# Performance work log

Hardware: AMD Instinct MI355X
Metric: run time of the kernel (lower is better)

Reference implementation:

```python
import jax, jax.numpy as jnp
import numpy as np

N, E = 50000, 800000
F_IN, F_OUT, H = 128, 16, 8
NEG_SLOPE = 0.2  # PyG GATConv default
EPS = 1e-5       # LayerNorm eps


def setup_inputs() -> dict:
    key = jax.random.key(0)
    ks = jax.random.split(key, 8)
    x = jax.random.normal(ks[0], (N, F_IN), dtype=jnp.float32)
    edge_index = jax.random.randint(ks[1], (2, E), 0, N, dtype=jnp.int32)
    s_in = 1.0 / np.sqrt(F_IN)
    s_f = 1.0 / np.sqrt(F_OUT)
    W = jax.random.normal(ks[2], (F_IN, H * F_OUT), dtype=jnp.float32) * s_in
    att_src = jax.random.normal(ks[3], (H, F_OUT), dtype=jnp.float32) * s_f
    att_dst = jax.random.normal(ks[4], (H, F_OUT), dtype=jnp.float32) * s_f
    bias = jnp.zeros((H * F_OUT,), dtype=jnp.float32)
    gamma = jnp.ones((H * F_OUT,), dtype=jnp.float32)
    beta = jnp.zeros((H * F_OUT,), dtype=jnp.float32)
    return {"x": x, "edge_index": edge_index, "W": W, "att_src": att_src,
            "att_dst": att_dst, "bias": bias, "gamma": gamma, "beta": beta}


def _gat_layer(x, edge_index, W, att_src, att_dst, bias, gamma, beta):
    n = x.shape[0]
    # add self loops (PyG GATConv default add_self_loops=True)
    loop = jnp.arange(n, dtype=edge_index.dtype)
    src = jnp.concatenate([edge_index[0], loop])  # message source j
    dst = jnp.concatenate([edge_index[1], loop])  # message target i

    xp = (x @ W).reshape(n, H, F_OUT)                      # [N,H,F]
    a_src = jnp.einsum('nhf,hf->nh', xp, att_src)          # [N,H]
    a_dst = jnp.einsum('nhf,hf->nh', xp, att_dst)          # [N,H]

    e = a_src[src] + a_dst[dst]                            # [E+N,H]
    e = jax.nn.leaky_relu(e, NEG_SLOPE)
    # softmax over incoming edges per destination node
    m = jax.ops.segment_max(e, dst, num_segments=n)        # [N,H]
    e = jnp.exp(e - m[dst])
    z = jax.ops.segment_sum(e, dst, num_segments=n)        # [N,H]
    alpha = e / jnp.where(z[dst] > 0, z[dst], 1.0)         # [E+N,H]

    msg = alpha[:, :, None] * xp[src]                      # [E+N,H,F]
    out = jax.ops.segment_sum(msg, dst, num_segments=n)    # [N,H,F]
    out = out.reshape(n, H * F_OUT) + bias

    # LayerNorm over feature dim
    mu = out.mean(axis=-1, keepdims=True)
    var = out.var(axis=-1, keepdims=True)
    return (out - mu) * jax.lax.rsqrt(var + EPS) * gamma + beta


def reference(x, edge_index, W, att_src, att_dst, bias, gamma, beta):
    return _gat_layer(x, edge_index, W, att_src, att_dst, bias, gamma, beta)
```

## Files before the change

kernel.cpp:

```cpp
#include <hip/hip_runtime.h>
#include <math.h>

#define F_IN 128
#define NHD 8
#define FEAT 128
#define NEG_SLOPE 0.2f
#define LN_EPS 1e-5f
#define BSH 7
#define BMSK 127
#define NPQ 32
#define CAP 48
#define EPB 2048
#define NBMAX 512

typedef __bf16 v8bf __attribute__((ext_vector_type(8)));
typedef __bf16 v2bf __attribute__((ext_vector_type(2)));
typedef float f32x4 __attribute__((ext_vector_type(4)));

__global__ __launch_bounds__(256) void k_wt(const float* __restrict__ W,
                                            __bf16* __restrict__ WT) {
    int idx = blockIdx.x * 256 + threadIdx.x;
    int k = idx >> 7, c = idx & 127;
    WT[c * 128 + k] = (__bf16)W[idx];
}

__global__ __launch_bounds__(512) void k_fused(const float* __restrict__ x,
                                               const __bf16* __restrict__ WT,
                                               const float* __restrict__ att_src,
                                               const float* __restrict__ att_dst,
                                               __bf16* __restrict__ xp16,
                                               float* __restrict__ a_src,
                                               float* __restrict__ a_dst,
                                               const int* __restrict__ src,
                                               const int* __restrict__ dst,
                                               unsigned int* __restrict__ sorted_g,
                                               int* __restrict__ runptr,
                                               int n, int E, int Ga) {
    __shared__ __bf16 xs[32][136];
    if ((int)blockIdx.x < Ga) {
        __shared__ int lcnt[NBMAX];
        __shared__ int loff[NBMAX + 1];
        __shared__ unsigned int sorted_l[EPB];
        __shared__ int wtot[8], wexcl[8];
        int NB = (n + BMSK) >> BSH;
        int tid = threadIdx.x, lane = tid & 63, wid = tid >> 6;
        long base0 = (long)blockIdx.x * EPB;
        long total = (long)E + n;
        if (tid < NB) lcnt[tid] = 0;
        __syncthreads();

        int s0[4], d0[4];
        bool val[4];
        long e0 = base0 + (long)tid * 4;
        if (e0 + 3 < E) {
            int4 sv = *(const int4*)(src + e0);
            int4 dv = *(const int4*)(dst + e0);
            s0[0] = sv.x; s0[1] = sv.y; s0[2] = sv.z; s0[3] = sv.w;
            d0[0] = dv.x; d0[1] = dv.y; d0[2] = dv.z; d0[3] = dv.w;
            val[0] = val[1] = val[2] = val[3] = true;
        } else {
#pragma unroll
            for (int j = 0; j < 4; ++j) {
                long e = e0 + j;
                val[j] = (e < total);
                s0[j] = d0[j] = 0;
                if (val[j]) {
                    if (e < E) { s0[j] = src[e]; d0[j] = dst[e]; }
                    else { s0[j] = d0[j] = (int)(e - E); }
                }
            }
        }
#pragma unroll
        for (int j = 0; j < 4; ++j)
            if (val[j]) atomicAdd(&lcnt[d0[j] >> BSH], 1);
        __syncthreads();

        int v = (tid < NB) ? lcnt[tid] : 0;
        int xx = v;
#pragma unroll
        for (int o = 1; o < 64; o <<= 1) {
            int t2 = __shfl_up(xx, o);
            if (lane >= o) xx += t2;
        }
        if (lane == 63) wtot[wid] = xx;
        __syncthreads();
        if (wid == 0 && lane < 8) {
            int s = wtot[lane];
            int y = s;
#pragma unroll
            for (int o = 1; o < 8; o <<= 1) {
                int t2 = __shfl_up(y, o);
                if (lane >= o) y += t2;
            }
            wexcl[lane] = y - s;
        }
        __syncthreads();
        int excl = wexcl[wid] + xx - v;
        if (tid < NB) loff[tid] = excl;
        if (tid == NB - 1) loff[NB] = excl + v;
        __syncthreads();
        if (tid < NB) lcnt[tid] = loff[tid];
        __syncthreads();
#pragma unroll
        for (int j = 0; j < 4; ++j) {
            if (val[j]) {
                int b = d0[j] >> BSH;
                int pos = atomicAdd(&lcnt[b], 1);
                sorted_l[pos] = ((unsigned)s0[j] << BSH) | (unsigned)(d0[j] & BMSK);
            }
        }
        __syncthreads();
        int tv = loff[NB];
        for (int i = tid; i < tv; i += 512)
            sorted_g[base0 + i] = sorted_l[i];
        if (tid <= NB) runptr[(long)blockIdx.x * (NBMAX + 1) + tid] = loff[tid];
    } else {
        int gb = blockIdx.x - Ga;
        int tid = threadIdx.x;
        int rowbase = gb * 32;
        {
            int i4 = tid;
#pragma unroll
            for (int rep = 0; rep < 2; ++rep, i4 += 512) {
                int r = i4 >> 5, c4 = i4 & 31;
                int gr = rowbase + r; if (gr > n - 1) gr = n - 1;
                float4 xv = *(const float4*)(x + (long)gr * 128 + c4 * 4);
                __bf16* p = &xs[r][c4 * 4];
                p[0] = (__bf16)xv.x; p[1] = (__bf16)xv.y;
                p[2] = (__bf16)xv.z; p[3] = (__bf16)xv.w;
            }
        }
        __syncthreads();
        int wv = tid >> 6;
        int lane = tid & 63;
        int m = lane & 15, quad = lane >> 4;
        int colbase = wv * 16;
        const __bf16* wcol = WT + (colbase + m) * 128;
        v8bf wf[4];
#pragma unroll
        for (int kk = 0; kk < 4; ++kk)
            wf[kk] = *(const v8bf*)(wcol + kk * 32 + quad * 8);
        float ws = att_src[colbase + m];
        float wd = att_dst[colbase + m];
#pragma unroll
        for (int t = 0; t < 2; ++t) {
            int rb = t * 16;
            f32x4 acc = {0.f, 0.f, 0.f, 0.f};
#pragma unroll
            for (int kk = 0; kk < 4; ++kk) {
                v8bf a = *(const v8bf*)(&xs[rb + m][kk * 32 + quad * 8]);
                acc = __builtin_amdgcn_mfma_f32_16x16x32_bf16(a, wf[kk], acc, 0, 0, 0);
            }
#pragma unroll
            for (int r = 0; r < 4; ++r) {
                int row = rowbase + rb + quad * 4 + r;
                float ts = acc[r] * ws;
                float td = acc[r] * wd;
#pragma unroll
                for (int o = 1; o < 16; o <<= 1) {
                    ts += __shfl_xor(ts, o);
                    td += __shfl_xor(td, o);
                }
                if (row < n) {
                    xp16[(long)row * 128 + colbase + m] = (__bf16)acc[r];
                    if (m == 0) {
                        a_src[row * 8 + wv] = ts;
                        a_dst[row * 8 + wv] = td;
                    }
                }
            }
        }
    }
}

__global__ __launch_bounds__(256) void k_ba(const unsigned int* __restrict__ sorted_g,
                                            const int* __restrict__ runptr,
                                            const float* __restrict__ a_src,
                                            const float* __restrict__ a_dst,
                                            const __bf16* __restrict__ xp16,
                                            const float* __restrict__ bias,
                                            const float* __restrict__ gamma,
                                            const float* __restrict__ beta,
                                            const int* __restrict__ src,
                                            const int* __restrict__ dst,
                                            float* __restrict__ out, int n, int E, int Ga) {
    __shared__ int slds[NPQ * CAP];
    __shared__ int lc[NPQ];
    __shared__ float adst_s[NPQ * NHD];
    int b = blockIdx.x >> 2;
    int q = blockIdx.x & 3;
    int tid = threadIdx.x;
    int node0 = (b << BSH) + q * NPQ;
    if (tid < NPQ) lc[tid] = 0;
    if (tid < NPQ * NHD) {
        int nd = node0 + (tid >> 3);
        adst_s[tid] = (nd < n) ? a_dst[nd * NHD + (tid & 7)] : 0.f;
    }
    __syncthreads();

    int qlo = q * NPQ;
    for (int blk = tid; blk < Ga; blk += 256) {
        const int* rp = runptr + (long)blk * (NBMAX + 1) + b;
        int st = rp[0], en = rp[1];
        const unsigned int* sg = sorted_g + (long)blk * EPB;
        for (int i = st; i < en; ++i) {
            unsigned int u = sg[i];
            int dl = (int)(u & BMSK) - qlo;
            if ((unsigned)dl < NPQ) {
                int p = atomicAdd(&lc[dl], 1);
                if (p < CAP) slds[dl * CAP + p] = (int)(u >> BSH);
            }
        }
    }
    __syncthreads();
    if (tid < NPQ) {
        int cc = lc[tid]; if (cc > CAP) cc = CAP;
        int pad = (cc + 7) & ~7; if (pad > CAP) pad = CAP;
        for (int p = cc; p < pad; ++p) slds[tid * CAP + p] = 0;
    }
    __syncthreads();

    int lane = tid & 63, wv = tid >> 6;
    int h = lane & 7, j8 = lane >> 3;
    float2 bs = *(const float2*)(bias + 2 * lane);
    float2 g  = *(const float2*)(gamma + 2 * lane);
    float2 bt = *(const float2*)(beta + 2 * lane);

    for (int i = wv; i < NPQ; i += 4) {
        int node = node0 + i;
        if (node >= n) break;
        int cnt = lc[i];
        float acc0 = 0.f, acc1 = 0.f, inv;

        if (cnt <= CAP) {
            const int* row = slds + i * CAP;
            float b_h = adst_s[i * NHD + h];
            float zacc = 0.f;
            for (int base = 0; base < cnt; base += 8) {
                int s_my = row[base + j8];
                float e = a_src[s_my * NHD + h] + b_h;
                e = e > 0.f ? e : NEG_SLOPE * e;
                float w_my = (base + j8 < cnt) ? __expf(e) : 0.f;
                zacc += w_my;
                int ss[8];
#pragma unroll
                for (int j = 0; j < 8; ++j) ss[j] = row[base + j];
                float2 vals[8];
#pragma unroll
                for (int j = 0; j < 8; ++j) {
                    v2bf p = *(const v2bf*)(xp16 + (long)ss[j] * FEAT + 2 * lane);
                    vals[j] = make_float2((float)p[0], (float)p[1]);
                }
#pragma unroll
                for (int j = 0; j < 8; ++j) {
                    float w = __shfl(w_my, j * 8 + j8);
                    acc0 = fmaf(w, vals[j].x, acc0);
                    acc1 = fmaf(w, vals[j].y, acc1);
                }
            }
            zacc += __shfl_xor(zacc, 8);
            zacc += __shfl_xor(zacc, 16);
            zacc += __shfl_xor(zacc, 32);
            float z = __shfl(zacc, j8);
            inv = 1.f / z;
        } else {
            float b_h = a_dst[node * NHD + j8];
            float z = 0.f;
            {
                float e = a_src[node * NHD + j8] + b_h;
                e = e > 0.f ? e : NEG_SLOPE * e;
                float w = __expf(e);
                z += w;
                v2bf p = *(const v2bf*)(xp16 + (long)node * FEAT + 2 * lane);
                acc0 = fmaf(w, (float)p[0], acc0);
                acc1 = fmaf(w, (float)p[1], acc1);
            }
            for (int base = 0; base < E; base += 64) {
                int e = base + lane;
                int sv = 0;
                bool mt = false;
                if (e < E) { mt = (dst[e] == node); if (mt) sv = src[e]; }
                unsigned long long mask = __ballot(mt);
                while (mask) {
                    int bl = __ffsll(mask) - 1;
                    mask &= mask - 1;
                    int s = __shfl(sv, bl);
                    float ee = a_src[s * NHD + j8] + b_h;
                    ee = ee > 0.f ? ee : NEG_SLOPE * ee;
                    float w = __expf(ee);
                    z += w;
                    v2bf p = *(const v2bf*)(xp16 + (long)s * FEAT + 2 * lane);
                    acc0 = fmaf(w, (float)p[0], acc0);
                    acc1 = fmaf(w, (float)p[1], acc1);
                }
            }
            inv = 1.f / z;
        }

        float v0 = acc0 * inv + bs.x;
        float v1 = acc1 * inv + bs.y;
        float ssum = v0 + v1;
        float ssq = v0 * v0 + v1 * v1;
#pragma unroll
        for (int o = 32; o > 0; o >>= 1) {
            ssum += __shfl_xor(ssum, o);
            ssq += __shfl_xor(ssq, o);
        }
        float mu = ssum * (1.0f / FEAT);
        float var = ssq * (1.0f / FEAT) - mu * mu;
        float rs = rsqrtf(var + LN_EPS);
        float2 o2;
        o2.x = (v0 - mu) * rs * g.x + bt.x;
        o2.y = (v1 - mu) * rs * g.y + bt.y;
        *(float2*)(out + (long)node * FEAT + 2 * lane) = o2;
    }
}

extern "C" void kernel_launch(void* const* d_in, const int* in_sizes, int n_in,
                              void* d_out, int out_size, void* d_ws, size_t ws_size,
                              hipStream_t stream) {
    const float* x = (const float*)d_in[0];
    const int* edge_index = (const int*)d_in[1];
    const float* W = (const float*)d_in[2];
    const float* att_src = (const float*)d_in[3];
    const float* att_dst = (const float*)d_in[4];
    const float* bias = (const float*)d_in[5];
    const float* gamma = (const float*)d_in[6];
    const float* beta = (const float*)d_in[7];
    float* out = (float*)d_out;

    int n = in_sizes[0] / F_IN;
    int E = in_sizes[1] / 2;
    const int* src = edge_index;
    const int* dst = edge_index + E;
    int NB = (n + BMSK) >> BSH;
    int Ga = (E + n + EPB - 1) / EPB;

    char* ws = (char*)d_ws;
    __bf16* WT   = (__bf16*)ws;                    ws += (size_t)128 * 128 * 2;
    __bf16* xp16 = (__bf16*)ws;                    ws += (size_t)n * FEAT * 2;
    float* a_src = (float*)ws;                     ws += (size_t)n * NHD * 4;
    float* a_dst = (float*)ws;                     ws += (size_t)n * NHD * 4;
    unsigned int* sorted_g = (unsigned int*)ws;    ws += (size_t)Ga * EPB * 4;
    int* runptr  = (int*)ws;                       ws += (size_t)Ga * (NBMAX + 1) * 4;

    k_wt<<<64, 256, 0, stream>>>(W, WT);
    int Gg = (n + 31) / 32;
    k_fused<<<Ga + Gg, 512, 0, stream>>>(x, WT, att_src, att_dst, xp16, a_src, a_dst,
                                         src, dst, sorted_g, runptr, n, E, Ga);
    k_ba<<<NB * 4, 256, 0, stream>>>(sorted_g, runptr, a_src, a_dst, xp16,
                                     bias, gamma, beta, src, dst, out, n, E, Ga);
}
```

Baseline: 180.9 us.

## Stage GEMM output in LDS, widen row tiles, split aggregation blocks finer

The projection part of the fused kernel now handles 64 rows per block and stages the bf16 result in shared memory. From there it writes xp16 with coalesced 16-byte stores and computes the attention dot products directly, replacing the per-element strided stores and shuffle reductions. The aggregation kernel halves nodes per block (NPQ 16, 8 quarters per bucket) for more parallelism. It also precomputes all edge weights and a_src gathers up front, so the loads are independent of each other. The costs are more blocks each rescanning runptr, which doubles the bucket-scan traffic, and higher register use from the unrolled arrays.

```diff
diff --git a/kernel.cpp b/kernel.cpp
--- a/kernel.cpp
+++ b/kernel.cpp
@@ -8,10 +8,11 @@
 #define LN_EPS 1e-5f
 #define BSH 7
 #define BMSK 127
-#define NPQ 32
+#define NPQ 16
 #define CAP 48
 #define EPB 2048
 #define NBMAX 512
+#define GROWS 64
 
 typedef __bf16 v8bf __attribute__((ext_vector_type(8)));
 typedef __bf16 v2bf __attribute__((ext_vector_type(2)));
@@ -36,12 +37,13 @@
                                                unsigned int* __restrict__ sorted_g,
                                                int* __restrict__ runptr,
                                                int n, int E, int Ga) {
-    __shared__ __bf16 xs[32][136];
+    extern __shared__ char smem[];
     if ((int)blockIdx.x < Ga) {
-        __shared__ int lcnt[NBMAX];
-        __shared__ int loff[NBMAX + 1];
-        __shared__ unsigned int sorted_l[EPB];
-        __shared__ int wtot[8], wexcl[8];
+        int* lcnt = (int*)smem;
+        int* loff = lcnt + NBMAX;
+        unsigned int* sorted_l = (unsigned int*)(loff + NBMAX + 1);
+        int* wtot = (int*)(sorted_l + EPB);
+        int* wexcl = wtot + 8;
         int NB = (n + BMSK) >> BSH;
         int tid = threadIdx.x, lane = tid & 63, wid = tid >> 6;
         long base0 = (long)blockIdx.x * EPB;
@@ -115,24 +117,23 @@
             sorted_g[base0 + i] = sorted_l[i];
         if (tid <= NB) runptr[(long)blockIdx.x * (NBMAX + 1) + tid] = loff[tid];
     } else {
+        __bf16* xs = (__bf16*)smem;
+        __bf16* ys = xs + GROWS * 136;
         int gb = blockIdx.x - Ga;
         int tid = threadIdx.x;
-        int rowbase = gb * 32;
-        {
-            int i4 = tid;
-#pragma unroll
-            for (int rep = 0; rep < 2; ++rep, i4 += 512) {
-                int r = i4 >> 5, c4 = i4 & 31;
-                int gr = rowbase + r; if (gr > n - 1) gr = n - 1;
-                float4 xv = *(const float4*)(x + (long)gr * 128 + c4 * 4);
-                __bf16* p = &xs[r][c4 * 4];
-                p[0] = (__bf16)xv.x; p[1] = (__bf16)xv.y;
-                p[2] = (__bf16)xv.z; p[3] = (__bf16)xv.w;
-            }
-        }
-        __syncthreads();
-        int wv = tid >> 6;
-        int lane = tid & 63;
+        int rowbase = gb * GROWS;
+#pragma unroll
+        for (int rep = 0; rep < 4; ++rep) {
+            int i4 = tid + rep * 512;
+            int r = i4 >> 5, c4 = i4 & 31;
+            int gr = rowbase + r; if (gr > n - 1) gr = n - 1;
+            float4 xv = *(const float4*)(x + (long)gr * 128 + c4 * 4);
+            __bf16* p = xs + r * 136 + c4 * 4;
+            p[0] = (__bf16)xv.x; p[1] = (__bf16)xv.y;
+            p[2] = (__bf16)xv.z; p[3] = (__bf16)xv.w;
+        }
+        __syncthreads();
+        int wv = tid >> 6, lane = tid & 63;
         int m = lane & 15, quad = lane >> 4;
         int colbase = wv * 16;
         const __bf16* wcol = WT + (colbase + m) * 128;
@@ -140,34 +141,46 @@
 #pragma unroll
         for (int kk = 0; kk < 4; ++kk)
             wf[kk] = *(const v8bf*)(wcol + kk * 32 + quad * 8);
-        float ws = att_src[colbase + m];
-        float wd = att_dst[colbase + m];
-#pragma unroll
-        for (int t = 0; t < 2; ++t) {
+#pragma unroll
+        for (int t = 0; t < 4; ++t) {
             int rb = t * 16;
             f32x4 acc = {0.f, 0.f, 0.f, 0.f};
 #pragma unroll
             for (int kk = 0; kk < 4; ++kk) {
-                v8bf a = *(const v8bf*)(&xs[rb + m][kk * 32 + quad * 8]);
+                v8bf a = *(const v8bf*)(xs + (rb + m) * 136 + kk * 32 + quad * 8);
                 acc = __builtin_amdgcn_mfma_f32_16x16x32_bf16(a, wf[kk], acc, 0, 0, 0);
             }
 #pragma unroll
-            for (int r = 0; r < 4; ++r) {
-                int row = rowbase + rb + quad * 4 + r;
-                float ts = acc[r] * ws;
-                float td = acc[r] * wd;
-#pragma unroll
-                for (int o = 1; o < 16; o <<= 1) {
-                    ts += __shfl_xor(ts, o);
-                    td += __shfl_xor(td, o);
-                }
-                if (row < n) {
-                    xp16[(long)row * 128 + colbase + m] = (__bf16)acc[r];
-                    if (m == 0) {
-                        a_src[row * 8 + wv] = ts;
-                        a_dst[row * 8 + wv] = td;
-                    }
-                }
+            for (int r = 0; r < 4; ++r)
+                ys[(rb + quad * 4 + r) * 136 + colbase + m] = (__bf16)acc[r];
+        }
+        __syncthreads();
+#pragma unroll
+        for (int rep = 0; rep < 2; ++rep) {
+            int i8 = tid + rep * 512;
+            int r = i8 >> 4, c8 = i8 & 15;
+            int gr = rowbase + r;
+            if (gr < n)
+                *(v8bf*)(xp16 + (long)gr * 128 + c8 * 8) = *(v8bf*)(ys + r * 136 + c8 * 8);
+        }
+        {
+            int r = tid >> 3, h = tid & 7;
+            int gr = rowbase + r;
+            if (gr < n) {
+                const __bf16* yr = ys + r * 136 + h * 16;
+                v8bf y0 = *(const v8bf*)yr;
+                v8bf y1 = *(const v8bf*)(yr + 8);
+                const float* as = att_src + h * 16;
+                const float* ad = att_dst + h * 16;
+                float ts = 0.f, td = 0.f;
+#pragma unroll
+                for (int k = 0; k < 8; ++k) {
+                    float v0 = (float)y0[k], v1 = (float)y1[k];
+                    ts += v0 * as[k] + v1 * as[k + 8];
+                    td += v0 * ad[k] + v1 * ad[k + 8];
+                }
+                a_src[gr * 8 + h] = ts;
+                a_dst[gr * 8 + h] = td;
             }
         }
     }
@@ -187,8 +200,8 @@
     __shared__ int slds[NPQ * CAP];
     __shared__ int lc[NPQ];
     __shared__ float adst_s[NPQ * NHD];
-    int b = blockIdx.x >> 2;
-    int q = blockIdx.x & 3;
+    int b = blockIdx.x >> 3;
+    int q = blockIdx.x & 7;
     int tid = threadIdx.x;
     int node0 = (b << BSH) + q * NPQ;
     if (tid < NPQ) lc[tid] = 0;
@@ -235,34 +248,45 @@
         if (cnt <= CAP) {
             const int* row = slds + i * CAP;
             float b_h = adst_s[i * NHD + h];
+            int C = (cnt + 7) >> 3;
+            int smy[6]; float av[6], w_all[6];
+#pragma unroll
+            for (int c = 0; c < 6; ++c) if (c < C) smy[c] = row[c * 8 + j8];
+#pragma unroll
+            for (int c = 0; c < 6; ++c) if (c < C) av[c] = a_src[smy[c] * NHD + h];
             float zacc = 0.f;
-            for (int base = 0; base < cnt; base += 8) {
-                int s_my = row[base + j8];
-                float e = a_src[s_my * NHD + h] + b_h;
+#pragma unroll
+            for (int c = 0; c < 6; ++c) if (c < C) {
+                float e = av[c] + b_h;
                 e = e > 0.f ? e : NEG_SLOPE * e;
-                float w_my = (base + j8 < cnt) ? __expf(e) : 0.f;
-                zacc += w_my;
-                int ss[8];
-#pragma unroll
-                for (int j = 0; j < 8; ++j) ss[j] = row[base + j];
-                float2 vals[8];
-#pragma unroll
-                for (int j = 0; j < 8; ++j) {
-                    v2bf p = *(const v2bf*)(xp16 + (long)ss[j] * FEAT + 2 * lane);
-                    vals[j] = make_float2((float)p[0], (float)p[1]);
-                }
-#pragma unroll
-                for (int j = 0; j < 8; ++j) {
-                    float w = __shfl(w_my, j * 8 + j8);
-                    acc0 = fmaf(w, vals[j].x, acc0);
-                    acc1 = fmaf(w, vals[j].y, acc1);
-                }
+                float w = (c * 8 + j8 < cnt) ? __expf(e) : 0.f;
+                w_all[c] = w;
+                zacc += w;
             }
             zacc += __shfl_xor(zacc, 8);
             zacc += __shfl_xor(zacc, 16);
             zacc += __shfl_xor(zacc, 32);
             float z = __shfl(zacc, j8);
             inv = 1.f / z;
+#pragma unroll
+            for (int c = 0; c < 6; ++c) if (c < C) {
+                int base = c * 8;
+                int ss[8];
+#pragma unroll
+                for (int j = 0; j < 8; ++j) ss[j] = row[base + j];
+                float2 vals[8];
+#pragma unroll
+                for (int j = 0; j < 8; ++j) {
+                    v2bf p = *(const v2bf*)(xp16 + (long)ss[j] * FEAT + 2 * lane);
+                    vals[j] = make_float2((float)p[0], (float)p[1]);
+                }
+#pragma unroll
+                for (int j = 0; j < 8; ++j) {
+                    float w = __shfl(w_all[c], j * 8 + j8);
+                    acc0 = fmaf(w, vals[j].x, acc0);
+                    acc1 = fmaf(w, vals[j].y, acc1);
+                }
+            }
         } else {
             float b_h = a_dst[node * NHD + j8];
             float z = 0.f;
@@ -345,9 +369,10 @@
     int* runptr  = (int*)ws;                       ws += (size_t)Ga * (NBMAX + 1) * 4;
 
     k_wt<<<64, 256, 0, stream>>>(W, WT);
-    int Gg = (n + 31) / 32;
-    k_fused<<<Ga + Gg, 512, 0, stream>>>(x, WT, att_src, att_dst, xp16, a_src, a_dst,
-                                         src, dst, sorted_g, runptr, n, E, Ga);
-    k_ba<<<NB * 4, 256, 0, stream>>>(sorted_g, runptr, a_src, a_dst, xp16,
+    int Gg = (n + GROWS - 1) / GROWS;
+    size_t smem = (size_t)GROWS * 136 * 2 * 2;
+    k_fused<<<Ga + Gg, 512, smem, stream>>>(x, WT, att_src, att_dst, xp16, a_src, a_dst,
+                                            src, dst, sorted_g, runptr, n, E, Ga);
+    k_ba<<<NB * 8, 256, 0, stream>>>(sorted_g, runptr, a_src, a_dst, xp16,
                                      bias, gamma, beta, src, dst, out, n, E, Ga);
 }
```

Result: slower. 221.2 us (+22.3%).
